# Kernel tuning notes

Measured on AMD Instinct MI355X. Metric: run time of the kernel, lower is better.

## Reference

```python
import jax, jax.numpy as jnp
import numpy as np


def setup_inputs() -> dict:
    key = jax.random.key(0)
    k1, k2, k3 = jax.random.split(key, 3)
    B, D, G = 128, 1024, 40
    x = jax.random.normal(k1, (B, D), dtype=jnp.float32)
    g = jax.random.randint(k2, (B,), 0, 100, dtype=jnp.int64)
    layer_transform_0 = jax.random.normal(k3, (G, D, D), dtype=jnp.float32)
    return {"x": x, "g": g, "layer_transform_0": layer_transform_0, "l": 0, "n": 1}


def reference(x, g, layer_transform_0, l, n):
    # l selects which layer transform table; only one table here (layer_sizes=[1024]).
    # n is unused by the original forward.
    G = layer_transform_0.shape[0]
    shape = x.shape
    xf = x.reshape(shape[0], -1)               # (B, D)
    idx = g % G                                 # (B,)
    T = layer_transform_0[idx]                  # (B, D, D) gathered per-sample matrices
    out = jnp.einsum('bd,bde->be', xf, T)       # batched matvec (M=1 bmm)
    return out.reshape(shape)
```

## Files before the change

kernel.cpp:

```cpp
#include <hip/hip_runtime.h>


#define B_DIM   128
#define D_DIM   1024
#define G_DIM   40
#define SMAX    8
#define ECH     16
#define ECOLS   64
#define DSL     16
#define THREADS 256

typedef float f4 __attribute__((ext_vector_type(4)));

__global__ __launch_bounds__(THREADS) void leqfc_fused(
    const float* __restrict__ x,
    const int* __restrict__ g,
    const float* __restrict__ T,
    float* __restrict__ out)
{
    const int gi  = blockIdx.x;
    const int e0  = blockIdx.y * ECOLS;
    const int tid = threadIdx.x;
    const int sl  = tid >> 4;
    const int eth = tid & 15;

    __shared__ float smem[SMAX * D_DIM];
    __shared__ int   mem[B_DIM];
    __shared__ int   cnt;

    if (tid == 0) cnt = 0;
    __syncthreads();
    if (tid < B_DIM) {
        if ((g[tid] % G_DIM) == gi)
            mem[atomicAdd(&cnt, 1)] = tid;
    }
    __syncthreads();
    const int m = cnt;

    const f4* __restrict__ x4 = reinterpret_cast<const f4*>(x);
    const f4* __restrict__ Tp = reinterpret_cast<const f4*>(
        T + (size_t)gi * D_DIM * D_DIM + (size_t)(sl * 64) * D_DIM + e0) + eth;
    f4* smem4 = reinterpret_cast<f4*>(smem);

    for (int s0 = 0; s0 < m; s0 += SMAX) {
        const int mc = min(SMAX, m - s0);

        __syncthreads();
        #pragma unroll
        for (int k = 0; k < 8; ++k) {
            const int fq = tid + k * THREADS;
            const int j  = fq >> 8;
            const int dq = fq & 255;
            smem4[fq] = (j < mc) ? x4[(size_t)mem[s0 + j] * (D_DIM / 4) + dq]
                                 : (f4)(0.f);
        }
        __syncthreads();

        f4 acc[SMAX];
        #pragma unroll
        for (int j = 0; j < SMAX; ++j) acc[j] = (f4)(0.f);

        #pragma unroll 4
        for (int k = 0; k < 16; ++k) {
            const f4 t0 = __builtin_nontemporal_load(&Tp[(size_t)(4 * k + 0) * (D_DIM / 4)]);
            const f4 t1 = __builtin_nontemporal_load(&Tp[(size_t)(4 * k + 1) * (D_DIM / 4)]);
            const f4 t2 = __builtin_nontemporal_load(&Tp[(size_t)(4 * k + 2) * (D_DIM / 4)]);
            const f4 t3 = __builtin_nontemporal_load(&Tp[(size_t)(4 * k + 3) * (D_DIM / 4)]);
            const int dq = sl * 16 + k;
            #pragma unroll
            for (int j = 0; j < SMAX; ++j) {
                const f4 xv = smem4[j * (D_DIM / 4) + dq];
                acc[j].x = fmaf(xv.x, t0.x, fmaf(xv.y, t1.x, fmaf(xv.z, t2.x, fmaf(xv.w, t3.x, acc[j].x))));
                acc[j].y = fmaf(xv.x, t0.y, fmaf(xv.y, t1.y, fmaf(xv.z, t2.y, fmaf(xv.w, t3.y, acc[j].y))));
                acc[j].z = fmaf(xv.x, t0.z, fmaf(xv.y, t1.z, fmaf(xv.z, t2.z, fmaf(xv.w, t3.z, acc[j].z))));
                acc[j].w = fmaf(xv.x, t0.w, fmaf(xv.y, t1.w, fmaf(xv.z, t2.w, fmaf(xv.w, t3.w, acc[j].w))));
            }
        }

        __syncthreads();
        #pragma unroll
        for (int j = 0; j < SMAX; ++j)
            smem4[(j * DSL + sl) * (ECOLS / 4) + eth] = acc[j];
        __syncthreads();

        #pragma unroll
        for (int o2 = 0; o2 < 2; ++o2) {
            const int o = tid + o2 * THREADS;
            const int j = o >> 6;
            const int c = o & 63;
            if (j < mc) {
                float s = 0.f;
                #pragma unroll
                for (int ss = 0; ss < DSL; ++ss)
                    s += smem[(j * DSL + ss) * ECOLS + c];
                __builtin_nontemporal_store(
                    s, &out[(size_t)mem[s0 + j] * D_DIM + e0 + c]);
            }
        }
    }
}

extern "C" void kernel_launch(void* const* d_in, const int* in_sizes, int n_in,
                              void* d_out, int out_size, void* d_ws, size_t ws_size,
                              hipStream_t stream)
{
    const float* x = (const float*)d_in[0];
    const int*   g = (const int*)d_in[1];
    const float* T = (const float*)d_in[2];
    float* out = (float*)d_out;

    dim3 grid(G_DIM, ECH);
    leqfc_fused<<<grid, THREADS, 0, stream>>>(x, g, T, out);
}
```

Measured before the change: 30.54 us.

## Split reduction dimension across two blocks with workspace partials and reduce kernel

Splits the D reduction dimension into two halves along a new grid z-axis, doubling the block count (to 1280) so more of the GPU streams T concurrently. Each block writes partial sums to a workspace, and a second kernel adds the two halves into the output. The intra-block reduction now uses wave shuffles plus a small shared buffer instead of a full shared-memory transpose. The cost is an extra kernel launch and an extra 1 MB write and read of partials.

```diff
diff --git a/kernel.cpp b/kernel.cpp
--- a/kernel.cpp
+++ b/kernel.cpp
@@ -7,24 +7,28 @@
 #define SMAX    8
 #define ECH     16
 #define ECOLS   64
-#define DSL     16
+#define DHALF   512
+#define NSL     16
 #define THREADS 256
 
 typedef float f4 __attribute__((ext_vector_type(4)));
 
-__global__ __launch_bounds__(THREADS) void leqfc_fused(
+__global__ __launch_bounds__(THREADS) void leqfc_main(
     const float* __restrict__ x,
     const int* __restrict__ g,
     const float* __restrict__ T,
-    float* __restrict__ out)
+    float* __restrict__ part)
 {
     const int gi  = blockIdx.x;
     const int e0  = blockIdx.y * ECOLS;
+    const int dh  = blockIdx.z;
+    const int d0  = dh * DHALF;
     const int tid = threadIdx.x;
     const int sl  = tid >> 4;
     const int eth = tid & 15;
 
-    __shared__ float smem[SMAX * D_DIM];
+    __shared__ float xs[SMAX * DHALF];
+    __shared__ f4    red[SMAX * 4 * 16];
     __shared__ int   mem[B_DIM];
     __shared__ int   cnt;
 
@@ -39,20 +43,24 @@
 
     const f4* __restrict__ x4 = reinterpret_cast<const f4*>(x);
     const f4* __restrict__ Tp = reinterpret_cast<const f4*>(
-        T + (size_t)gi * D_DIM * D_DIM + (size_t)(sl * 64) * D_DIM + e0) + eth;
-    f4* smem4 = reinterpret_cast<f4*>(smem);
+        T + (size_t)gi * D_DIM * D_DIM + (size_t)(d0 + sl * 32) * D_DIM + e0) + eth;
+    f4* xs4 = reinterpret_cast<f4*>(xs);
+
+    const int wv = tid >> 6;
+    const int ln = tid & 63;
 
     for (int s0 = 0; s0 < m; s0 += SMAX) {
         const int mc = min(SMAX, m - s0);
 
         __syncthreads();
         #pragma unroll
-        for (int k = 0; k < 8; ++k) {
+        for (int k = 0; k < 4; ++k) {
             const int fq = tid + k * THREADS;
-            const int j  = fq >> 8;
-            const int dq = fq & 255;
-            smem4[fq] = (j < mc) ? x4[(size_t)mem[s0 + j] * (D_DIM / 4) + dq]
-                                 : (f4)(0.f);
+            const int j  = fq >> 7;
+            const int dq = fq & 127;
+            xs4[fq] = (j < mc)
+                ? x4[(size_t)mem[s0 + j] * (D_DIM / 4) + dh * (DHALF / 4) + dq]
+                : (f4)(0.f);
         }
         __syncthreads();
 
@@ -61,15 +69,15 @@
         for (int j = 0; j < SMAX; ++j) acc[j] = (f4)(0.f);
 
         #pragma unroll 4
-        for (int k = 0; k < 16; ++k) {
+        for (int k = 0; k < 8; ++k) {
             const f4 t0 = __builtin_nontemporal_load(&Tp[(size_t)(4 * k + 0) * (D_DIM / 4)]);
             const f4 t1 = __builtin_nontemporal_load(&Tp[(size_t)(4 * k + 1) * (D_DIM / 4)]);
             const f4 t2 = __builtin_nontemporal_load(&Tp[(size_t)(4 * k + 2) * (D_DIM / 4)]);
             const f4 t3 = __builtin_nontemporal_load(&Tp[(size_t)(4 * k + 3) * (D_DIM / 4)]);
-            const int dq = sl * 16 + k;
+            const int dq = sl * 8 + k;
             #pragma unroll
             for (int j = 0; j < SMAX; ++j) {
-                const f4 xv = smem4[j * (D_DIM / 4) + dq];
+                const f4 xv = xs4[j * (DHALF / 4) + dq];
                 acc[j].x = fmaf(xv.x, t0.x, fmaf(xv.y, t1.x, fmaf(xv.z, t2.x, fmaf(xv.w, t3.x, acc[j].x))));
                 acc[j].y = fmaf(xv.x, t0.y, fmaf(xv.y, t1.y, fmaf(xv.z, t2.y, fmaf(xv.w, t3.y, acc[j].y))));
                 acc[j].z = fmaf(xv.x, t0.z, fmaf(xv.y, t1.z, fmaf(xv.z, t2.z, fmaf(xv.w, t3.z, acc[j].z))));
@@ -77,27 +85,51 @@
             }
         }
 
-        __syncthreads();
         #pragma unroll
-        for (int j = 0; j < SMAX; ++j)
-            smem4[(j * DSL + sl) * (ECOLS / 4) + eth] = acc[j];
+        for (int j = 0; j < SMAX; ++j) {
+            #pragma unroll
+            for (int c = 0; c < 4; ++c) {
+                float v = acc[j][c];
+                v += __shfl_xor(v, 16);
+                v += __shfl_xor(v, 32);
+                acc[j][c] = v;
+            }
+        }
+        if (ln < 16) {
+            #pragma unroll
+            for (int j = 0; j < SMAX; ++j)
+                red[(j * 4 + wv) * 16 + ln] = acc[j];
+        }
         __syncthreads();
 
-        #pragma unroll
-        for (int o2 = 0; o2 < 2; ++o2) {
-            const int o = tid + o2 * THREADS;
-            const int j = o >> 6;
-            const int c = o & 63;
+        if (tid < SMAX * 16) {
+            const int j = tid >> 4;
+            const int e = tid & 15;
             if (j < mc) {
-                float s = 0.f;
+                f4 s = red[(j * 4 + 0) * 16 + e];
                 #pragma unroll
-                for (int ss = 0; ss < DSL; ++ss)
-                    s += smem[(j * DSL + ss) * ECOLS + c];
-                __builtin_nontemporal_store(
-                    s, &out[(size_t)mem[s0 + j] * D_DIM + e0 + c]);
+                for (int w = 1; w < 4; ++w) {
+                    const f4 v = red[(j * 4 + w) * 16 + e];
+                    s.x += v.x; s.y += v.y; s.z += v.z; s.w += v.w;
+                }
+                f4* o = reinterpret_cast<f4*>(
+                    part + ((size_t)dh * B_DIM + mem[s0 + j]) * D_DIM + e0) + e;
+                *o = s;
             }
         }
+        __syncthreads();
     }
+}
+
+__global__ __launch_bounds__(256) void leqfc_reduce(
+    const float* __restrict__ part, float* __restrict__ out)
+{
+    const int idx = blockIdx.x * 256 + threadIdx.x;
+    const f4* p4 = reinterpret_cast<const f4*>(part);
+    const f4 a = p4[idx];
+    const f4 b = p4[(size_t)(B_DIM * D_DIM / 4) + idx];
+    f4 s; s.x = a.x + b.x; s.y = a.y + b.y; s.z = a.z + b.z; s.w = a.w + b.w;
+    __builtin_nontemporal_store(s, &reinterpret_cast<f4*>(out)[idx]);
 }
 
 extern "C" void kernel_launch(void* const* d_in, const int* in_sizes, int n_in,
@@ -107,8 +139,10 @@
     const float* x = (const float*)d_in[0];
     const int*   g = (const int*)d_in[1];
     const float* T = (const float*)d_in[2];
-    float* out = (float*)d_out;
+    float* out  = (float*)d_out;
+    float* part = (float*)d_ws;
 
-    dim3 grid(G_DIM, ECH);
-    leqfc_fused<<<grid, THREADS, 0, stream>>>(x, g, T, out);
+    dim3 grid(G_DIM, ECH, 2);
+    leqfc_main<<<grid, THREADS, 0, stream>>>(x, g, T, part);
+    leqfc_reduce<<<(B_DIM * D_DIM / 4) / 256, 256, 0, stream>>>(part, out);
 }
```

After: 38.14 us. 24.9% more time.
